# Kernel tuning notes

Hardware: AMD Instinct MI355X
Metric: run time of the kernel (lower is better)

## Reference

```python
import jax, jax.numpy as jnp
import numpy as np

BOUND = 1.0
DENSITY_SCALE = 1.0
MIN_NEAR = 0.2
EPS = 1e-15


def setup_inputs() -> dict:
    key = jax.random.key(0)
    ks = jax.random.split(key, 10)
    N, H = 32768, 32
    rays_o = (jax.random.uniform(ks[0], (N, 3), jnp.float32) - 0.5)  # inside AABB
    rays_d = jax.random.normal(ks[1], (N, 3), jnp.float32)
    W1 = jax.random.normal(ks[2], (3, H), jnp.float32) * 0.5
    b1 = jnp.zeros((H,), jnp.float32)
    Wsig = jax.random.normal(ks[3], (H, 1), jnp.float32) * 0.5
    Wsig_d = jax.random.normal(ks[4], (H, 1), jnp.float32) * 0.5
    Wc1 = jax.random.normal(ks[5], (6, H), jnp.float32) * 0.5
    bc1 = jnp.zeros((H,), jnp.float32)
    Wc2 = jax.random.normal(ks[6], (H, 3), jnp.float32) * 0.5
    Wc2_d = jax.random.normal(ks[7], (H, 3), jnp.float32) * 0.5
    return {"rays_o": rays_o, "rays_d": rays_d, "W1": W1, "b1": b1,
            "Wsig": Wsig, "Wsig_d": Wsig_d, "Wc1": Wc1, "bc1": bc1,
            "Wc2": Wc2, "Wc2_d": Wc2_d, "num_steps": 128}


def _composite(deltas, sigma, z01, rgbs):
    # alphas / transmittance / weights, as in run()
    alphas = 1.0 - jnp.exp(-deltas * DENSITY_SCALE * sigma)           # [N,T]
    shifted = jnp.concatenate([jnp.ones_like(alphas[..., :1]),
                               1.0 - alphas + EPS], axis=-1)
    weights = alphas * jnp.cumprod(shifted, axis=-1)[..., :-1]        # [N,T]
    ws = weights.sum(axis=-1)                                          # [N]
    depth = jnp.sum(weights * z01, axis=-1)                            # [N]
    image = jnp.sum(weights[..., None] * rgbs, axis=-2)                # [N,3]
    image = image + (1.0 - ws)[..., None] * 1.0  # bg_color = 1
    return image, depth, ws


def reference(rays_o, rays_d, W1, b1, Wsig, Wsig_d, Wc1, bc1, Wc2, Wc2_d, num_steps):
    N = rays_o.shape[0]
    T = num_steps
    d = rays_d / jnp.linalg.norm(rays_d, axis=-1, keepdims=True)
    # near_far_from_aabb (slab test), aabb = [-1,1]^3
    inv = 1.0 / d
    t1 = (-BOUND - rays_o) * inv
    t2 = (BOUND - rays_o) * inv
    near = jnp.max(jnp.minimum(t1, t2), axis=-1, keepdims=True)        # [N,1]
    far = jnp.min(jnp.maximum(t1, t2), axis=-1, keepdims=True)
    near = jnp.maximum(near, MIN_NEAR)
    far = jnp.maximum(far, near + 1e-6)
    z = jnp.linspace(0.0, 1.0, T, dtype=rays_o.dtype)[None, :]
    z_vals = near + (far - near) * z                                    # [N,T]
    sample_dist = (far - near) / T                                      # [N,1]
    xyzs = rays_o[:, None, :] + d[:, None, :] * z_vals[..., None]       # [N,T,3]
    xyzs = jnp.clip(xyzs, -BOUND, BOUND)
    # surrogate density MLP (shared trunk, main + dummy heads)
    h = jax.nn.relu(jnp.einsum('ntc,ch->nth', xyzs, W1) + b1)           # [N,T,H]
    sigma = jax.nn.softplus(jnp.einsum('nth,ho->nt', h, Wsig))          # [N,T]
    sigma_dummy = jax.nn.softplus(jnp.einsum('nth,ho->nt', h, Wsig_d))
    # deltas
    deltas = z_vals[..., 1:] - z_vals[..., :-1]
    deltas = jnp.concatenate([deltas, sample_dist * jnp.ones_like(deltas[..., :1])], axis=-1)
    # surrogate color MLP on (xyz, dir)
    dirs = jnp.broadcast_to(d[:, None, :], xyzs.shape)
    feat = jnp.concatenate([xyzs, dirs], axis=-1)                       # [N,T,6]
    hc = jax.nn.relu(jnp.einsum('ntc,ch->nth', feat, Wc1) + bc1)
    rgbs = jax.nn.sigmoid(jnp.einsum('nth,hc->ntc', hc, Wc2))           # [N,T,3]
    rgbs_dummy = jax.nn.sigmoid(jnp.einsum('nth,hc->ntc', hc, Wc2_d))
    z01 = jnp.clip((z_vals - near) / (far - near), 0.0, 1.0)
    image, depth, ws = _composite(deltas, sigma, z01, rgbs)
    image_d, depth_d, _ = _composite(deltas, sigma_dummy, z01, rgbs_dummy)
    # pack: image(3) | depth(1) | weights_sum(1) | image_dummy(3) | depth_dummy(1)
    return jnp.concatenate([image, depth[:, None], ws[:, None],
                            image_d, depth_d[:, None]], axis=-1)        # [N,9]
```

## Files before the change

### kernel.cpp

```cpp
#include <hip/hip_runtime.h>
#include <hip/hip_bf16.h>


typedef float  f32x4  __attribute__((ext_vector_type(4)));
typedef short  bf16x8 __attribute__((ext_vector_type(8)));
typedef unsigned int u32;

__device__ __forceinline__ float fast_rcp(float x){ return __builtin_amdgcn_rcpf(x); }
__device__ __forceinline__ float softplus_f(float x){
    float e = __expf(-fabsf(x));
    return fmaxf(x,0.f) + __logf(1.f+e);
}
__device__ __forceinline__ float sigmoid_f(float x){ return fast_rcp(1.f+__expf(-x)); }

__device__ __forceinline__ u32 pkrn(float lo, float hi){
    const u32 a = __float_as_uint(lo) + 0x8000u;
    const u32 b = __float_as_uint(hi) + 0x8000u;
    return __builtin_amdgcn_perm(b, a, 0x07060302u);
}
__device__ __forceinline__ u32 bfr_hi(float f){
    u32 u = __float_as_uint(f);
    return (u + 0x7FFFu + ((u>>16)&1u)) & 0xFFFF0000u;
}
__device__ __forceinline__ u32 pkbf(float lo, float hi){
    return (bfr_hi(lo)>>16) | bfr_hi(hi);
}

__global__ __launch_bounds__(256)
void nerf_prep_kernel(const float* __restrict__ W1, const float* __restrict__ b1,
                      const float* __restrict__ Wsig, const float* __restrict__ Wsig_d,
                      const float* __restrict__ Wc1, const float* __restrict__ bc1,
                      const float* __restrict__ Wc2, const float* __restrict__ Wc2_d,
                      u32* __restrict__ ws)
{
    const int q0 = threadIdx.x;
#pragma unroll
    for (int k = 0; k < 6; ++k) {
        const int q = q0 + k*256;
        u32 val = 0u;
        if (q < 1024) {
            const int ut = q>>8, rem = q&255, lane = rem>>2, dw = rem&3;
            const int g = lane>>4, m = lane&15;
            if (g == 0) {
                float w[8];
                if (ut < 2) { const int u = ut*16 + m;
                    w[0]=W1[u];  w[1]=W1[32+u];  w[2]=W1[64+u];  w[3]=b1[u];
                    w[4]=0.f;    w[5]=0.f;       w[6]=0.f;       w[7]=0.f;
                } else {        const int u = (ut-2)*16 + m;
                    w[0]=Wc1[u]; w[1]=Wc1[32+u]; w[2]=Wc1[64+u]; w[3]=bc1[u];
                    w[4]=Wc1[96+u]; w[5]=Wc1[128+u]; w[6]=Wc1[160+u]; w[7]=0.f;
                }
                val = pkbf(w[2*dw], w[2*dw+1]);
            }
        } else {
            const int q2 = q-1024, ch = q2>>8, rem = q2&255, lane = rem>>2, dw = rem&3;
            const int g = lane>>4, o = lane&15;
            float w[2];
#pragma unroll
            for (int e = 0; e < 2; ++e) {
                const int kk = 2*dw + e;
                const int h = kk>>2, rr = kk&3;
                const int u_local = h*16 + g*4 + rr;
                float v = 0.f;
                if (ch == 0) {
                    if (o == 0) v = Wsig[u_local];
                    else if (o == 1) v = Wsig_d[u_local];
                } else {
                    if (o >= 2 && o <= 4) v = Wc2[u_local*3 + (o-2)];
                    else if (o >= 5 && o <= 7) v = Wc2_d[u_local*3 + (o-5)];
                }
                w[e] = v;
            }
            val = pkbf(w[0], w[1]);
        }
        ws[q] = val;
    }
}

#define PSTR 8
#define SSTR 20
#define WSTR 1792
#define CSTR 52
#define PART_OFF 2048

__global__ __launch_bounds__(256, 5)
void nerf_render_kernel(const float* __restrict__ rays_o,
                        const float* __restrict__ rays_d,
                        const u32*  __restrict__ wsm,
                        const int*  __restrict__ num_steps,
                        float* __restrict__ partials,
                        int N)
{
    __shared__ u32 smem[4 * WSTR];

    const int tid  = threadIdx.x;
    const int seg  = tid>>6, lane = tid&63;
    const int half = blockIdx.x & 1;
    const int ray  = (blockIdx.x >> 1)*64 + lane;
    const int rayc = (ray < N) ? ray : (N-1);
    const int T = num_steps[0];
    const int g = lane>>4, c = lane&15;

    u32*   posW   = smem + seg*WSTR;
    float* stashW = (float*)(smem + seg*WSTR + 64*PSTR);
    float* comb   = (float*)smem;

    const uint4* wsv = (const uint4*)wsm;
    uint4 a1u0 = wsv[0*64 + lane];
    uint4 a1u1 = wsv[1*64 + lane];
    uint4 a1u2 = wsv[2*64 + lane];
    uint4 a1u3 = wsv[3*64 + lane];
    uint4 a2u0 = wsv[256 + 0*64 + lane];
    uint4 a2u1 = wsv[256 + 1*64 + lane];
    asm volatile("" : "+v"(a1u0.x), "+v"(a1u0.y), "+v"(a1u0.z), "+v"(a1u0.w),
                      "+v"(a1u1.x), "+v"(a1u1.y), "+v"(a1u1.z), "+v"(a1u1.w),
                      "+v"(a1u2.x), "+v"(a1u2.y), "+v"(a1u2.z), "+v"(a1u2.w));
    asm volatile("" : "+v"(a1u3.x), "+v"(a1u3.y), "+v"(a1u3.z), "+v"(a1u3.w),
                      "+v"(a2u0.x), "+v"(a2u0.y), "+v"(a2u0.z), "+v"(a2u0.w),
                      "+v"(a2u1.x), "+v"(a2u1.y), "+v"(a2u1.z), "+v"(a2u1.w));

    const float ox = rays_o[rayc*3+0], oy = rays_o[rayc*3+1], oz = rays_o[rayc*3+2];
    const float rdx = rays_d[rayc*3+0], rdy = rays_d[rayc*3+1], rdz = rays_d[rayc*3+2];
    const float rn = rsqrtf(rdx*rdx + rdy*rdy + rdz*rdz);
    const float dx = rdx*rn, dy = rdy*rn, dz = rdz*rn;

    const float ix = 1.0f/dx, iy = 1.0f/dy, iz = 1.0f/dz;
    const float t1x = (-1.f-ox)*ix, t2x = (1.f-ox)*ix;
    const float t1y = (-1.f-oy)*iy, t2y = (1.f-oy)*iy;
    const float t1z = (-1.f-oz)*iz, t2z = (1.f-oz)*iz;
    float nearv = fmaxf(fmaxf(fminf(t1x,t2x), fminf(t1y,t2y)), fminf(t1z,t2z));
    float farv  = fminf(fminf(fmaxf(t1x,t2x), fmaxf(t1y,t2y)), fmaxf(t1z,t2z));
    nearv = fmaxf(nearv, 0.2f);
    farv  = fmaxf(farv, nearv + 1e-6f);

    const float span    = farv - nearv;
    const float stepz   = (T > 1) ? span/(float)(T-1) : 0.f;
    const float inv_tm1 = (T > 1) ? 1.f/(float)(T-1) : 0.f;
    const float last_dt = span/(float)T;

    const u32 dirw0 = pkbf(dx, dy);
    const u32 dirw1 = pkbf(dz, 0.f);

    const int halfT = (T + 1) >> 1;
    const int Sper  = (halfT + 3) >> 2;
    const int hEnd  = ((half + 1)*halfT < T) ? (half + 1)*halfT : T;
    const int segStart = half*halfT + seg*Sper;
    int segEnd = segStart + Sper;
    segEnd = (segEnd < hEnd) ? segEnd : hEnd;
    const int nch = (segEnd > segStart) ? ((segEnd - segStart + 1) >> 1) : 0;

    const int posOff = 4*c;
    const int stOff  = (c>>1)*SSTR + (c&1)*8 + g*4;

    float iA0=0.f,iA1=0.f,iA2=0.f,dAc=0.f,wsA=0.f,TAx=1.f;
    float iD0=0.f,iD1=0.f,iD2=0.f,dDc=0.f,wsD=0.f,TDx=1.f;
    const f32x4 z4 = {0.f,0.f,0.f,0.f};

    for (int cs = 0; cs < nch; ++cs) {
        const int t0 = segStart + cs*2;

#pragma unroll
        for (int i = 0; i < 2; ++i) {
            const float zv = fmaf(stepz, (float)(t0 + i), nearv);
            const float X = fminf(fmaxf(fmaf(dx, zv, ox), -1.f), 1.f);
            const float Y = fminf(fmaxf(fmaf(dy, zv, oy), -1.f), 1.f);
            const float Z = fminf(fmaxf(fmaf(dz, zv, oz), -1.f), 1.f);
            uint4 v;
            v.x = pkrn(X, Y);
            v.y = pkrn(Z, 1.0f);
            v.z = dirw0;
            v.w = dirw1;
            *(uint4*)&posW[lane*PSTR + i*4] = v;
        }

#define TILEB(TAU)                                                                \
        {                                                                         \
            const uint4 b1u = *(const uint4*)&posW[(TAU)*(8*PSTR) + posOff];      \
            const bf16x8 b1f = __builtin_bit_cast(bf16x8, b1u);                   \
            f32x4 acc10 = __builtin_amdgcn_mfma_f32_16x16x32_bf16(                \
                __builtin_bit_cast(bf16x8, a1u0), b1f, z4, 0,0,0);                \
            f32x4 acc11 = __builtin_amdgcn_mfma_f32_16x16x32_bf16(                \
                __builtin_bit_cast(bf16x8, a1u1), b1f, z4, 0,0,0);                \
            f32x4 acc12 = __builtin_amdgcn_mfma_f32_16x16x32_bf16(                \
                __builtin_bit_cast(bf16x8, a1u2), b1f, z4, 0,0,0);                \
            f32x4 acc13 = __builtin_amdgcn_mfma_f32_16x16x32_bf16(                \
                __builtin_bit_cast(bf16x8, a1u3), b1f, z4, 0,0,0);                \
            const f32x4 r0 = __builtin_elementwise_max(acc10, z4);                \
            const f32x4 r1 = __builtin_elementwise_max(acc11, z4);                \
            const f32x4 r2 = __builtin_elementwise_max(acc12, z4);                \
            const f32x4 r3 = __builtin_elementwise_max(acc13, z4);                \
            uint4 b2a, b2b;                                                       \
            b2a.x = pkrn(r0.x, r0.y);  b2a.y = pkrn(r0.z, r0.w);                  \
            b2a.z = pkrn(r1.x, r1.y);  b2a.w = pkrn(r1.z, r1.w);                  \
            b2b.x = pkrn(r2.x, r2.y);  b2b.y = pkrn(r2.z, r2.w);                  \
            b2b.z = pkrn(r3.x, r3.y);  b2b.w = pkrn(r3.z, r3.w);                  \
            f32x4 acc2 = __builtin_amdgcn_mfma_f32_16x16x32_bf16(                 \
                __builtin_bit_cast(bf16x8, a2u0), __builtin_bit_cast(bf16x8, b2a),\
                z4, 0, 0, 0);                                                     \
            acc2 = __builtin_amdgcn_mfma_f32_16x16x32_bf16(                       \
                __builtin_bit_cast(bf16x8, a2u1), __builtin_bit_cast(bf16x8, b2b),\
                acc2, 0, 0, 0);                                                   \
            if (g < 2) {                                                          \
                *(f32x4*)&stashW[(TAU)*(8*SSTR) + stOff] = acc2;                  \
            }                                                                     \
        }
        TILEB(0) TILEB(1) TILEB(2) TILEB(3)
        TILEB(4) TILEB(5) TILEB(6) TILEB(7)
#undef TILEB

#pragma unroll
        for (int t = 0; t < 2; ++t) {
            const int tg = t0 + t;
            if (tg < segEnd) {
                const f32x4 oA = *(const f32x4*)&stashW[lane*SSTR + t*8];
                const f32x4 oB = *(const f32x4*)&stashW[lane*SSTR + t*8 + 4];
                const float dneg = (tg < T-1) ? -stepz : -last_dt;
                const float z01  = (float)tg * inv_tm1;

                const float sigA = softplus_f(oA.x);
                const float qA = __expf(dneg*sigA);
                const float wA = TAx - TAx*qA; TAx *= qA;
                iA0 = fmaf(wA, sigmoid_f(oA.z), iA0);
                iA1 = fmaf(wA, sigmoid_f(oA.w), iA1);
                iA2 = fmaf(wA, sigmoid_f(oB.x), iA2);
                dAc = fmaf(wA, z01, dAc); wsA += wA;

                const float sigD = softplus_f(oA.y);
                const float qD = __expf(dneg*sigD);
                const float wD = TDx - TDx*qD; TDx *= qD;
                iD0 = fmaf(wD, sigmoid_f(oB.y), iD0);
                iD1 = fmaf(wD, sigmoid_f(oB.z), iD1);
                iD2 = fmaf(wD, sigmoid_f(oB.w), iD2);
                dDc = fmaf(wD, z01, dDc); wsD += wD;
            }
        }
    }

    __syncthreads();
    *(f32x4*)&comb[lane*CSTR + seg*12 + 0] = (f32x4){iA0, iA1, iA2, dAc};
    *(f32x4*)&comb[lane*CSTR + seg*12 + 4] = (f32x4){wsA, TAx, iD0, iD1};
    *(f32x4*)&comb[lane*CSTR + seg*12 + 8] = (f32x4){iD2, dDc, wsD, TDx};
    __syncthreads();

    if (seg == 0 && ray < N) {
        float tA = TAx, tD = TDx;
#pragma unroll
        for (int s = 1; s < 4; ++s) {
            const f32x4 v0 = *(const f32x4*)&comb[lane*CSTR + s*12 + 0];
            const f32x4 v1 = *(const f32x4*)&comb[lane*CSTR + s*12 + 4];
            const f32x4 v2 = *(const f32x4*)&comb[lane*CSTR + s*12 + 8];
            iA0 = fmaf(tA, v0.x, iA0);
            iA1 = fmaf(tA, v0.y, iA1);
            iA2 = fmaf(tA, v0.z, iA2);
            dAc = fmaf(tA, v0.w, dAc);
            wsA = fmaf(tA, v1.x, wsA);
            tA *= v1.y;
            iD0 = fmaf(tD, v1.z, iD0);
            iD1 = fmaf(tD, v1.w, iD1);
            iD2 = fmaf(tD, v2.x, iD2);
            dDc = fmaf(tD, v2.y, dDc);
            wsD = fmaf(tD, v2.z, wsD);
            tD *= v2.w;
        }
        float* pw = partials + (size_t)(half*N + ray)*12;
        *(f32x4*)&pw[0] = (f32x4){iA0, iA1, iA2, dAc};
        *(f32x4*)&pw[4] = (f32x4){wsA, tA, iD0, iD1};
        *(f32x4*)&pw[8] = (f32x4){iD2, dDc, wsD, tD};
    }
}

__global__ __launch_bounds__(256)
void nerf_combine_kernel(const float* __restrict__ partials,
                         float* __restrict__ out, int N)
{
    const int ray = blockIdx.x*256 + threadIdx.x;
    if (ray >= N) return;
    const float* p0 = partials + (size_t)ray*12;
    const float* p1 = partials + (size_t)(N + ray)*12;
    const f32x4 a0 = *(const f32x4*)&p0[0];
    const f32x4 a1 = *(const f32x4*)&p0[4];
    const f32x4 a2 = *(const f32x4*)&p0[8];
    const f32x4 b0 = *(const f32x4*)&p1[0];
    const f32x4 b1 = *(const f32x4*)&p1[4];
    const f32x4 b2 = *(const f32x4*)&p1[8];

    const float TA0 = a1.y, TD0 = a2.w;
    const float iA0 = a0.x + TA0*b0.x;
    const float iA1 = a0.y + TA0*b0.y;
    const float iA2 = a0.z + TA0*b0.z;
    const float dAc = a0.w + TA0*b0.w;
    const float wsA = a1.x + TA0*b1.x;
    const float iD0 = a1.z + TD0*b1.z;
    const float iD1 = a1.w + TD0*b1.w;
    const float iD2 = a2.x + TD0*b2.x;
    const float dDc = a2.y + TD0*b2.y;
    const float wsD = a2.z + TD0*b2.z;

    const float bgA = 1.f - wsA;
    const float bgD = 1.f - wsD;
    float* o = out + (size_t)ray * 9;
    o[0] = iA0 + bgA;
    o[1] = iA1 + bgA;
    o[2] = iA2 + bgA;
    o[3] = dAc;
    o[4] = wsA;
    o[5] = iD0 + bgD;
    o[6] = iD1 + bgD;
    o[7] = iD2 + bgD;
    o[8] = dDc;
}

extern "C" void kernel_launch(void* const* d_in, const int* in_sizes, int n_in,
                              void* d_out, int out_size, void* d_ws, size_t ws_size,
                              hipStream_t stream) {
    const float* rays_o = (const float*)d_in[0];
    const float* rays_d = (const float*)d_in[1];
    const float* W1     = (const float*)d_in[2];
    const float* b1     = (const float*)d_in[3];
    const float* Wsig   = (const float*)d_in[4];
    const float* Wsig_d = (const float*)d_in[5];
    const float* Wc1    = (const float*)d_in[6];
    const float* bc1    = (const float*)d_in[7];
    const float* Wc2    = (const float*)d_in[8];
    const float* Wc2_d  = (const float*)d_in[9];
    const int* num_steps = (const int*)d_in[10];

    const int N = in_sizes[0] / 3;
    float* out = (float*)d_out;
    u32*   ws  = (u32*)d_ws;
    float* partials = (float*)((u32*)d_ws + PART_OFF);

    hipLaunchKernelGGL(nerf_prep_kernel, dim3(1), dim3(256), 0, stream,
                       W1, b1, Wsig, Wsig_d, Wc1, bc1, Wc2, Wc2_d, ws);

    const int rblocks = ((N + 63) / 64) * 2;
    hipLaunchKernelGGL(nerf_render_kernel, dim3(rblocks), dim3(256), 0, stream,
                       rays_o, rays_d, ws, num_steps, partials, N);

    const int cblocks = (N + 255) / 256;
    hipLaunchKernelGGL(nerf_combine_kernel, dim3(cblocks), dim3(256), 0, stream,
                       partials, out, N);
}
```

Baseline: 59.86 us.

## Split each ray's samples across eight waves and process one sample per iteration

The render block grows from 256 to 512 threads, so each ray's half of the samples is split across 8 wave segments instead of 4, and each iteration handles one sample instead of two. LDS strides and the final cross-segment combine are resized to match. Bf16 packing switches from round-to-nearest to truncation, and the exponentials now use exp2f with a LOG2E-prescaled step. MFMA sections are wrapped in s_setprio to favour matrix issue. The aim is more waves in flight to hide latency, at the cost of a longer serial combine step and slightly less accurate bf16 inputs.

```diff
diff --git a/kernel.cpp b/kernel.cpp
--- a/kernel.cpp
+++ b/kernel.cpp
@@ -13,10 +13,8 @@
 }
 __device__ __forceinline__ float sigmoid_f(float x){ return fast_rcp(1.f+__expf(-x)); }
 
-__device__ __forceinline__ u32 pkrn(float lo, float hi){
-    const u32 a = __float_as_uint(lo) + 0x8000u;
-    const u32 b = __float_as_uint(hi) + 0x8000u;
-    return __builtin_amdgcn_perm(b, a, 0x07060302u);
+__device__ __forceinline__ u32 pktr(float lo, float hi){
+    return __builtin_amdgcn_perm(__float_as_uint(hi), __float_as_uint(lo), 0x07060302u);
 }
 __device__ __forceinline__ u32 bfr_hi(float f){
     u32 u = __float_as_uint(f);
@@ -77,13 +75,14 @@
     }
 }
 
-#define PSTR 8
-#define SSTR 20
-#define WSTR 1792
-#define CSTR 52
+#define PSTR 4
+#define SSTR 12
+#define WSTR 1024
+#define CSTR 100
 #define PART_OFF 2048
-
-__global__ __launch_bounds__(256, 5)
+#define LOG2E 1.44269504088896340736f
+
+__global__ __launch_bounds__(512, 8)
 void nerf_render_kernel(const float* __restrict__ rays_o,
                         const float* __restrict__ rays_d,
                         const u32*  __restrict__ wsm,
@@ -91,7 +90,7 @@
                         float* __restrict__ partials,
                         int N)
 {
-    __shared__ u32 smem[4 * WSTR];
+    __shared__ u32 smem[8 * WSTR];
 
     const int tid  = threadIdx.x;
     const int seg  = tid>>6, lane = tid&63;
@@ -137,45 +136,47 @@
     const float stepz   = (T > 1) ? span/(float)(T-1) : 0.f;
     const float inv_tm1 = (T > 1) ? 1.f/(float)(T-1) : 0.f;
     const float last_dt = span/(float)T;
+    const float nStep2  = -stepz  * LOG2E;
+    const float nLast2  = -last_dt * LOG2E;
 
     const u32 dirw0 = pkbf(dx, dy);
     const u32 dirw1 = pkbf(dz, 0.f);
 
     const int halfT = (T + 1) >> 1;
-    const int Sper  = (halfT + 3) >> 2;
+    const int Sper  = (halfT + 7) >> 3;
     const int hEnd  = ((half + 1)*halfT < T) ? (half + 1)*halfT : T;
     const int segStart = half*halfT + seg*Sper;
     int segEnd = segStart + Sper;
     segEnd = (segEnd < hEnd) ? segEnd : hEnd;
-    const int nch = (segEnd > segStart) ? ((segEnd - segStart + 1) >> 1) : 0;
+    const int nch = (segEnd > segStart) ? (segEnd - segStart) : 0;
 
     const int posOff = 4*c;
-    const int stOff  = (c>>1)*SSTR + (c&1)*8 + g*4;
+    const int stOff  = c*SSTR + g*4;
 
     float iA0=0.f,iA1=0.f,iA2=0.f,dAc=0.f,wsA=0.f,TAx=1.f;
     float iD0=0.f,iD1=0.f,iD2=0.f,dDc=0.f,wsD=0.f,TDx=1.f;
     const f32x4 z4 = {0.f,0.f,0.f,0.f};
 
     for (int cs = 0; cs < nch; ++cs) {
-        const int t0 = segStart + cs*2;
-
-#pragma unroll
-        for (int i = 0; i < 2; ++i) {
-            const float zv = fmaf(stepz, (float)(t0 + i), nearv);
+        const int tg = segStart + cs;
+
+        {
+            const float zv = fmaf(stepz, (float)tg, nearv);
             const float X = fminf(fmaxf(fmaf(dx, zv, ox), -1.f), 1.f);
             const float Y = fminf(fmaxf(fmaf(dy, zv, oy), -1.f), 1.f);
             const float Z = fminf(fmaxf(fmaf(dz, zv, oz), -1.f), 1.f);
             uint4 v;
-            v.x = pkrn(X, Y);
-            v.y = pkrn(Z, 1.0f);
+            v.x = pktr(X, Y);
+            v.y = pktr(Z, 1.0f);
             v.z = dirw0;
             v.w = dirw1;
-            *(uint4*)&posW[lane*PSTR + i*4] = v;
-        }
-
+            *(uint4*)&posW[lane*PSTR] = v;
+        }
+
+        __builtin_amdgcn_s_setprio(1);
 #define TILEB(TAU)                                                                \
         {                                                                         \
-            const uint4 b1u = *(const uint4*)&posW[(TAU)*(8*PSTR) + posOff];      \
+            const uint4 b1u = *(const uint4*)&posW[(TAU)*(16*PSTR) + posOff];     \
             const bf16x8 b1f = __builtin_bit_cast(bf16x8, b1u);                   \
             f32x4 acc10 = __builtin_amdgcn_mfma_f32_16x16x32_bf16(                \
                 __builtin_bit_cast(bf16x8, a1u0), b1f, z4, 0,0,0);                \
@@ -190,10 +191,10 @@
             const f32x4 r2 = __builtin_elementwise_max(acc12, z4);                \
             const f32x4 r3 = __builtin_elementwise_max(acc13, z4);                \
             uint4 b2a, b2b;                                                       \
-            b2a.x = pkrn(r0.x, r0.y);  b2a.y = pkrn(r0.z, r0.w);                  \
-            b2a.z = pkrn(r1.x, r1.y);  b2a.w = pkrn(r1.z, r1.w);                  \
-            b2b.x = pkrn(r2.x, r2.y);  b2b.y = pkrn(r2.z, r2.w);                  \
-            b2b.z = pkrn(r3.x, r3.y);  b2b.w = pkrn(r3.z, r3.w);                  \
+            b2a.x = pktr(r0.x, r0.y);  b2a.y = pktr(r0.z, r0.w);                  \
+            b2a.z = pktr(r1.x, r1.y);  b2a.w = pktr(r1.z, r1.w);                  \
+            b2b.x = pktr(r2.x, r2.y);  b2b.y = pktr(r2.z, r2.w);                  \
+            b2b.z = pktr(r3.x, r3.y);  b2b.w = pktr(r3.z, r3.w);                  \
             f32x4 acc2 = __builtin_amdgcn_mfma_f32_16x16x32_bf16(                 \
                 __builtin_bit_cast(bf16x8, a2u0), __builtin_bit_cast(bf16x8, b2a),\
                 z4, 0, 0, 0);                                                     \
@@ -201,38 +202,34 @@
                 __builtin_bit_cast(bf16x8, a2u1), __builtin_bit_cast(bf16x8, b2b),\
                 acc2, 0, 0, 0);                                                   \
             if (g < 2) {                                                          \
-                *(f32x4*)&stashW[(TAU)*(8*SSTR) + stOff] = acc2;                  \
+                *(f32x4*)&stashW[(TAU)*(16*SSTR) + stOff] = acc2;                 \
             }                                                                     \
         }
         TILEB(0) TILEB(1) TILEB(2) TILEB(3)
-        TILEB(4) TILEB(5) TILEB(6) TILEB(7)
 #undef TILEB
-
-#pragma unroll
-        for (int t = 0; t < 2; ++t) {
-            const int tg = t0 + t;
-            if (tg < segEnd) {
-                const f32x4 oA = *(const f32x4*)&stashW[lane*SSTR + t*8];
-                const f32x4 oB = *(const f32x4*)&stashW[lane*SSTR + t*8 + 4];
-                const float dneg = (tg < T-1) ? -stepz : -last_dt;
-                const float z01  = (float)tg * inv_tm1;
-
-                const float sigA = softplus_f(oA.x);
-                const float qA = __expf(dneg*sigA);
-                const float wA = TAx - TAx*qA; TAx *= qA;
-                iA0 = fmaf(wA, sigmoid_f(oA.z), iA0);
-                iA1 = fmaf(wA, sigmoid_f(oA.w), iA1);
-                iA2 = fmaf(wA, sigmoid_f(oB.x), iA2);
-                dAc = fmaf(wA, z01, dAc); wsA += wA;
-
-                const float sigD = softplus_f(oA.y);
-                const float qD = __expf(dneg*sigD);
-                const float wD = TDx - TDx*qD; TDx *= qD;
-                iD0 = fmaf(wD, sigmoid_f(oB.y), iD0);
-                iD1 = fmaf(wD, sigmoid_f(oB.z), iD1);
-                iD2 = fmaf(wD, sigmoid_f(oB.w), iD2);
-                dDc = fmaf(wD, z01, dDc); wsD += wD;
-            }
+        __builtin_amdgcn_s_setprio(0);
+
+        {
+            const f32x4 oA = *(const f32x4*)&stashW[lane*SSTR];
+            const f32x4 oB = *(const f32x4*)&stashW[lane*SSTR + 4];
+            const float dneg2 = (tg < T-1) ? nStep2 : nLast2;
+            const float z01   = (float)tg * inv_tm1;
+
+            const float sigA = softplus_f(oA.x);
+            const float qA = exp2f(dneg2*sigA);
+            const float wA = TAx - TAx*qA; TAx *= qA;
+            iA0 = fmaf(wA, sigmoid_f(oA.z), iA0);
+            iA1 = fmaf(wA, sigmoid_f(oA.w), iA1);
+            iA2 = fmaf(wA, sigmoid_f(oB.x), iA2);
+            dAc = fmaf(wA, z01, dAc); wsA += wA;
+
+            const float sigD = softplus_f(oA.y);
+            const float qD = exp2f(dneg2*sigD);
+            const float wD = TDx - TDx*qD; TDx *= qD;
+            iD0 = fmaf(wD, sigmoid_f(oB.y), iD0);
+            iD1 = fmaf(wD, sigmoid_f(oB.z), iD1);
+            iD2 = fmaf(wD, sigmoid_f(oB.w), iD2);
+            dDc = fmaf(wD, z01, dDc); wsD += wD;
         }
     }
 
@@ -245,7 +242,7 @@
     if (seg == 0 && ray < N) {
         float tA = TAx, tD = TDx;
 #pragma unroll
-        for (int s = 1; s < 4; ++s) {
+        for (int s = 1; s < 8; ++s) {
             const f32x4 v0 = *(const f32x4*)&comb[lane*CSTR + s*12 + 0];
             const f32x4 v1 = *(const f32x4*)&comb[lane*CSTR + s*12 + 4];
             const f32x4 v2 = *(const f32x4*)&comb[lane*CSTR + s*12 + 8];
@@ -334,7 +331,7 @@
                        W1, b1, Wsig, Wsig_d, Wc1, bc1, Wc2, Wc2_d, ws);
 
     const int rblocks = ((N + 63) / 64) * 2;
-    hipLaunchKernelGGL(nerf_render_kernel, dim3(rblocks), dim3(256), 0, stream,
+    hipLaunchKernelGGL(nerf_render_kernel, dim3(rblocks), dim3(512), 0, stream,
                        rays_o, rays_d, ws, num_steps, partials, N);
 
     const int cblocks = (N + 255) / 256;
```

New measurement: 63.89 us. 1.07x slower.
